# Kernel optimization log

Hardware: AMD Instinct MI355X
Metric: run time of the kernel (lower is better)

## Reference

```python
import jax, jax.numpy as jnp
import numpy as np

ALPHA = 0.2  # tf.nn.leaky_relu default

def leaky(x):
    return jnp.where(x >= 0, x, ALPHA * x)

def segment_softmax(score, seg, num_segments):
    m = jax.ops.segment_max(score, seg, num_segments=num_segments)
    e = jnp.exp(score - m[seg])
    denom = jax.ops.segment_sum(e, seg, num_segments=num_segments)
    return e / denom[seg]

def setup_inputs() -> dict:
    key = jax.random.key(0)
    ks = jax.random.split(key, 8)
    E, NE, NR, D, U = 500000, 100000, 1000, 128, 128
    return {
        "h_index": jax.random.randint(ks[0], (E,), 0, NE),
        "r_index": jax.random.randint(ks[1], (E,), 0, NR),
        "t_index": jax.random.randint(ks[2], (E,), 0, NE),
        "entity_embeddings": jax.random.normal(ks[3], (NE, D), jnp.float32),
        "relation_embeddings": jax.random.normal(ks[4], (NR, D), jnp.float32),
        "W": jax.random.normal(ks[5], (3 * D, U), jnp.float32) * 0.05,
        "a": jax.random.normal(ks[6], (U, 1), jnp.float32) * 0.1,
        "a_b": jnp.zeros((1,), jnp.float32),
        "bias": jnp.zeros((U,), jnp.float32),
    }

def reference(h_index, r_index, t_index, entity_embeddings, relation_embeddings, W, a, a_b, bias):
    num_entities = entity_embeddings.shape[0]
    h = entity_embeddings[h_index]          # [E, D]
    r = relation_embeddings[r_index]        # [E, D]
    t = entity_embeddings[t_index]          # [E, D]
    feats = jnp.concatenate([h, r, t], axis=-1) @ W  # [E, U]
    # att_kernel Dense(1, activation=leaky_relu), then wrapped again in att_activation
    score = leaky(leaky(feats @ a + a_b))[:, 0]      # [E]
    alpha = segment_softmax(score, h_index, num_entities)
    msg = feats * alpha[:, None]                     # gcn_mapper: edge features * weight
    reduced = jax.ops.segment_sum(msg, h_index, num_segments=num_entities)  # [NE, U]
    out = reduced + bias                             # identity_updater returns reduced_msg
    return jax.nn.relu(out)
```

## Files before the change

kernel.cpp:

```cpp
#include <hip/hip_runtime.h>
#include <hip/hip_bf16.h>

#define ALPHA2 0.04f

typedef __attribute__((ext_vector_type(8))) short short8;
typedef __attribute__((ext_vector_type(4))) float floatx4;
typedef __attribute__((ext_vector_type(8))) unsigned short ushort8;

__device__ __forceinline__ unsigned short f2bf(float f) {
    unsigned u = __float_as_uint(f);
    unsigned r = (u + 0x7fffu + ((u >> 16) & 1u)) >> 16;
    return (unsigned short)r;
}
__device__ __forceinline__ float bf2f(unsigned short h) {
    return __uint_as_float((unsigned)h << 16);
}

__global__ void k_prep(const float* __restrict__ W, unsigned short* __restrict__ Wt,
                       int* __restrict__ count, int* __restrict__ cursor, int NE) {
    int idx = blockIdx.x * blockDim.x + threadIdx.x;
    if (idx < 384 * 128) {
        int k = idx >> 7, n = idx & 127;
        Wt[n * 384 + k] = f2bf(W[idx]);
    }
    if (idx < NE) { count[idx] = 0; cursor[idx] = 0; }
}

#define LDA 136

__device__ __forceinline__ void gemm_phase(
        const unsigned short* Ash, const unsigned short* Wsh,
        int rowbase, int nrows, int wave, int lane,
        const float* __restrict__ avec,
        unsigned short* __restrict__ OutB, float* __restrict__ svec) {
    int m16 = lane & 15, quad = lane >> 4;
    int rs = wave * 32;

    floatx4 acc[2][8];
    #pragma unroll
    for (int i = 0; i < 2; ++i)
        #pragma unroll
        for (int j = 0; j < 8; ++j) acc[i][j] = (floatx4){0.f, 0.f, 0.f, 0.f};

    #pragma unroll
    for (int kc = 0; kc < 4; ++kc) {
        short8 af[2], bf[8];
        #pragma unroll
        for (int i = 0; i < 2; ++i)
            af[i] = *(const short8*)(Ash + (rs + i * 16 + m16) * LDA + kc * 32 + quad * 8);
        #pragma unroll
        for (int j = 0; j < 8; ++j)
            bf[j] = *(const short8*)(Wsh + (j * 16 + m16) * LDA + kc * 32 + quad * 8);
        #pragma unroll
        for (int i = 0; i < 2; ++i)
            #pragma unroll
            for (int j = 0; j < 8; ++j)
                acc[i][j] = __builtin_amdgcn_mfma_f32_16x16x32_bf16(af[i], bf[j], acc[i][j], 0, 0, 0);
    }

    float av[8];
    #pragma unroll
    for (int j = 0; j < 8; ++j) av[j] = avec[j * 16 + m16];
    #pragma unroll
    for (int i = 0; i < 2; ++i) {
        #pragma unroll
        for (int reg = 0; reg < 4; ++reg) {
            int row = rowbase + rs + i * 16 + quad * 4 + reg;
            bool ok = row < nrows;
            float part = 0.f;
            #pragma unroll
            for (int j = 0; j < 8; ++j) {
                float v = acc[i][j][reg];
                part = fmaf(v, av[j], part);
                if (ok) OutB[(size_t)row * 128 + j * 16 + m16] = f2bf(v);
            }
            #pragma unroll
            for (int off = 1; off < 16; off <<= 1) part += __shfl_xor(part, off);
            if (ok && m16 == 0) svec[row] = part;
        }
    }
}

template <bool TWO>
__global__ __launch_bounds__(256) void k_gemm(
        const float* __restrict__ In,
        const unsigned short* __restrict__ Wt,
        int woffA, unsigned short* __restrict__ OutA, float* __restrict__ svecA,
        int woffB, unsigned short* __restrict__ OutB, float* __restrict__ svecB,
        int nrows, const float* __restrict__ avec) {
    __shared__ unsigned short Ash[128 * LDA];
    __shared__ unsigned short Wsh[128 * LDA];
    int tid = threadIdx.x;
    int rowbase = blockIdx.x * 128;
    int wave = tid >> 6, lane = tid & 63;

    #pragma unroll
    for (int it = 0; it < 16; ++it) {
        int id = it * 256 + tid;
        int chunk = id & 31, row = id >> 5;
        int grow = rowbase + row;
        if (grow > nrows - 1) grow = nrows - 1;
        float4 v = *(const float4*)(In + (size_t)grow * 128 + chunk * 4);
        ushort4 u = make_ushort4(f2bf(v.x), f2bf(v.y), f2bf(v.z), f2bf(v.w));
        *(ushort4*)(Ash + row * LDA + chunk * 4) = u;
    }
    #pragma unroll
    for (int it = 0; it < 8; ++it) {
        int id = it * 256 + tid;
        int chunk = id & 15, n = id >> 4;
        uint4 v = *(const uint4*)(Wt + (size_t)n * 384 + woffA + chunk * 8);
        *(uint4*)(Wsh + n * LDA + chunk * 8) = v;
    }
    __syncthreads();
    gemm_phase(Ash, Wsh, rowbase, nrows, wave, lane, avec, OutA, svecA);

    if (TWO) {
        __syncthreads();
        #pragma unroll
        for (int it = 0; it < 8; ++it) {
            int id = it * 256 + tid;
            int chunk = id & 15, n = id >> 4;
            uint4 v = *(const uint4*)(Wt + (size_t)n * 384 + woffB + chunk * 8);
            *(uint4*)(Wsh + n * LDA + chunk * 8) = v;
        }
        __syncthreads();
        gemm_phase(Ash, Wsh, rowbase, nrows, wave, lane, avec, OutB, svecB);
    }
}

__global__ void k_count(const int* __restrict__ h, int* __restrict__ count, int E) {
    int e = blockIdx.x * blockDim.x + threadIdx.x;
    if (e < E) atomicAdd(count + h[e], 1);
}

__device__ __forceinline__ int block_incl_scan256(int s, int* sh, int t) {
    sh[t] = s; __syncthreads();
    #pragma unroll
    for (int off = 1; off < 256; off <<= 1) {
        int x = 0;
        if (t >= off) x = sh[t - off];
        __syncthreads();
        sh[t] += x;
        __syncthreads();
    }
    return sh[t];
}

__global__ __launch_bounds__(256) void k_scan_a(const int* __restrict__ count, int NE,
                                                int* __restrict__ bsum) {
    __shared__ int sh[256];
    int b = blockIdx.x, t = threadIdx.x;
    int base = b * 1024 + t * 4, s = 0;
    #pragma unroll
    for (int j = 0; j < 4; ++j) { int i = base + j; if (i < NE) s += count[i]; }
    sh[t] = s; __syncthreads();
    for (int off = 128; off > 0; off >>= 1) {
        if (t < off) sh[t] += sh[t + off];
        __syncthreads();
    }
    if (t == 0) bsum[b] = sh[0];
}

__global__ __launch_bounds__(256) void k_scan_b(int* __restrict__ bsum, int NB) {
    __shared__ int sh[256];
    int t = threadIdx.x;
    int v[4]; int s = 0;
    #pragma unroll
    for (int j = 0; j < 4; ++j) { int i = t * 4 + j; v[j] = (i < NB) ? bsum[i] : 0; s += v[j]; }
    int incl = block_incl_scan256(s, sh, t);
    int excl = incl - s;
    #pragma unroll
    for (int j = 0; j < 4; ++j) {
        int i = t * 4 + j;
        if (i < NB) { int tmp = v[j]; bsum[i] = excl; excl += tmp; }
    }
}

__global__ __launch_bounds__(256) void k_scan_c(const int* __restrict__ count, int NE,
                                                const int* __restrict__ bsum,
                                                int* __restrict__ rowstart, int E) {
    __shared__ int sh[256];
    int b = blockIdx.x, t = threadIdx.x;
    int base = b * 1024 + t * 4;
    int v[4]; int s = 0;
    #pragma unroll
    for (int j = 0; j < 4; ++j) { int i = base + j; v[j] = (i < NE) ? count[i] : 0; s += v[j]; }
    int incl = block_incl_scan256(s, sh, t);
    int excl = bsum[b] + incl - s;
    #pragma unroll
    for (int j = 0; j < 4; ++j) {
        int i = base + j;
        if (i < NE) { rowstart[i] = excl; excl += v[j]; }
    }
    if (b == 0 && t == 0) rowstart[NE] = E;
}

__global__ void k_score_scatter(const int* __restrict__ h, const int* __restrict__ r,
                                const int* __restrict__ t, const float* __restrict__ s1,
                                const float* __restrict__ s2, const float* __restrict__ s3,
                                const float* __restrict__ a_b,
                                const int* __restrict__ rowstart, int* __restrict__ cursor,
                                uint2* __restrict__ rt_s, int E) {
    int e = blockIdx.x * blockDim.x + threadIdx.x;
    if (e >= E) return;
    int hi = h[e], ri = r[e], ti = t[e];
    float x = s1[hi] + s2[ri] + s3[ti] + a_b[0];
    float sc = (x >= 0.f) ? x : ALPHA2 * x;
    float ev = __expf(sc);
    int pos = atomicAdd(cursor + hi, 1);
    rt_s[rowstart[hi] + pos] = make_uint2(((unsigned)ri << 17) | (unsigned)ti,
                                          __float_as_uint(ev));
}

__global__ __launch_bounds__(256) void k_aggregate(const int* __restrict__ rowstart,
                                                   const uint2* __restrict__ rt_s,
                                                   const unsigned short* __restrict__ Pb,
                                                   const unsigned short* __restrict__ Qb,
                                                   const unsigned short* __restrict__ Rb,
                                                   const float* __restrict__ bias,
                                                   float* __restrict__ out, int NE) {
    int gid = blockIdx.x * blockDim.x + threadIdx.x;
    int n = gid >> 4;
    int sl = gid & 15;
    if (n >= NE) return;
    int start = rowstart[n], end = rowstart[n + 1];
    int c0 = sl * 8;
    float acc[8] = {};
    float evsum = 0.f;
    int i = start;
    for (; i + 2 <= end; i += 2) {
        uint2 m0 = rt_s[i], m1 = rt_s[i + 1];
        float ev0 = __uint_as_float(m0.y), ev1 = __uint_as_float(m1.y);
        unsigned t0 = m0.x & 0x1FFFFu, r0 = m0.x >> 17;
        unsigned t1 = m1.x & 0x1FFFFu, r1 = m1.x >> 17;
        ushort8 q0 = *(const ushort8*)(Qb + (size_t)t0 * 128 + c0);
        ushort8 rr0 = *(const ushort8*)(Rb + (size_t)r0 * 128 + c0);
        ushort8 q1 = *(const ushort8*)(Qb + (size_t)t1 * 128 + c0);
        ushort8 rr1 = *(const ushort8*)(Rb + (size_t)r1 * 128 + c0);
        evsum += ev0 + ev1;
        #pragma unroll
        for (int j = 0; j < 8; ++j)
            acc[j] = fmaf(ev0, bf2f(q0[j]) + bf2f(rr0[j]), acc[j]);
        #pragma unroll
        for (int j = 0; j < 8; ++j)
            acc[j] = fmaf(ev1, bf2f(q1[j]) + bf2f(rr1[j]), acc[j]);
    }
    if (i < end) {
        uint2 m0 = rt_s[i];
        float ev0 = __uint_as_float(m0.y);
        unsigned t0 = m0.x & 0x1FFFFu, r0 = m0.x >> 17;
        ushort8 q0 = *(const ushort8*)(Qb + (size_t)t0 * 128 + c0);
        ushort8 rr0 = *(const ushort8*)(Rb + (size_t)r0 * 128 + c0);
        evsum += ev0;
        #pragma unroll
        for (int j = 0; j < 8; ++j)
            acc[j] = fmaf(ev0, bf2f(q0[j]) + bf2f(rr0[j]), acc[j]);
    }
    float4 b0 = *(const float4*)(bias + c0);
    float4 b1 = *(const float4*)(bias + c0 + 4);
    float bi[8] = {b0.x, b0.y, b0.z, b0.w, b1.x, b1.y, b1.z, b1.w};
    float o[8];
    if (end > start) {
        float inv = 1.f / evsum;
        ushort8 pb = *(const ushort8*)(Pb + (size_t)n * 128 + c0);
        #pragma unroll
        for (int j = 0; j < 8; ++j) o[j] = bf2f(pb[j]) + acc[j] * inv + bi[j];
    } else {
        #pragma unroll
        for (int j = 0; j < 8; ++j) o[j] = bi[j];
    }
    #pragma unroll
    for (int j = 0; j < 8; ++j) o[j] = fmaxf(o[j], 0.f);
    float* op = out + (size_t)n * 128 + c0;
    *(float4*)(op)     = make_float4(o[0], o[1], o[2], o[3]);
    *(float4*)(op + 4) = make_float4(o[4], o[5], o[6], o[7]);
}

static inline size_t align_up(size_t x, size_t a) { return (x + a - 1) / a * a; }

extern "C" void kernel_launch(void* const* d_in, const int* in_sizes, int n_in,
                              void* d_out, int out_size, void* d_ws, size_t ws_size,
                              hipStream_t stream) {
    const int* h_index = (const int*)d_in[0];
    const int* r_index = (const int*)d_in[1];
    const int* t_index = (const int*)d_in[2];
    const float* ent = (const float*)d_in[3];
    const float* rel = (const float*)d_in[4];
    const float* W = (const float*)d_in[5];
    const float* a = (const float*)d_in[6];
    const float* a_b = (const float*)d_in[7];
    const float* bias = (const float*)d_in[8];
    float* out = (float*)d_out;

    int E = in_sizes[0];
    int NE = in_sizes[3] / 128;
    int NR = in_sizes[4] / 128;

    char* p = (char*)d_ws;
    auto alloc = [&](size_t bytes) { char* q = p; p += align_up(bytes, 256); return (void*)q; };
    unsigned short* Pb = (unsigned short*)alloc((size_t)NE * 128 * 2);
    unsigned short* Qb = (unsigned short*)alloc((size_t)NE * 128 * 2);
    unsigned short* Rb = (unsigned short*)alloc((size_t)NR * 128 * 2);
    unsigned short* Wt = (unsigned short*)alloc((size_t)128 * 384 * 2);
    float* s1 = (float*)alloc((size_t)NE * 4);
    float* s3 = (float*)alloc((size_t)NE * 4);
    float* s2 = (float*)alloc((size_t)NR * 4);
    int* count = (int*)alloc((size_t)NE * 4);
    int* cursor = (int*)alloc((size_t)NE * 4);
    int* rowstart = (int*)alloc((size_t)(NE + 1) * 4);
    int NB = (NE + 1023) / 1024;
    int* bsum = (int*)alloc((size_t)NB * 4);
    uint2* rt_s = (uint2*)alloc((size_t)E * 8);
    (void)ws_size; (void)n_in; (void)out_size;

    int nprep = (NE > 384 * 128) ? NE : 384 * 128;
    k_prep<<<(nprep + 255) / 256, 256, 0, stream>>>(W, Wt, count, cursor, NE);
    k_count<<<(E + 255) / 256, 256, 0, stream>>>(h_index, count, E);
    k_gemm<true><<<(NE + 127) / 128, 256, 0, stream>>>(ent, Wt, 0, Pb, s1, 256, Qb, s3, NE, a);
    k_gemm<false><<<(NR + 127) / 128, 256, 0, stream>>>(rel, Wt, 128, Rb, s2, 0, nullptr, nullptr, NR, a);
    k_scan_a<<<NB, 256, 0, stream>>>(count, NE, bsum);
    k_scan_b<<<1, 256, 0, stream>>>(bsum, NB);
    k_scan_c<<<NB, 256, 0, stream>>>(count, NE, bsum, rowstart, E);
    k_score_scatter<<<(E + 255) / 256, 256, 0, stream>>>(h_index, r_index, t_index,
                                                         s1, s2, s3, a_b, rowstart,
                                                         cursor, rt_s, E);
    k_aggregate<<<(NE * 16 + 255) / 256, 256, 0, stream>>>(rowstart, rt_s, Pb, Qb, Rb,
                                                           bias, out, NE);
}
```

Before: 230.8 us.

## Stage GEMM output through LDS for coalesced stores; record per-edge rank in count pass

Measured after the change: 216.5 us. 1.07x faster.

```diff
diff --git a/kernel.cpp b/kernel.cpp
--- a/kernel.cpp
+++ b/kernel.cpp
@@ -17,20 +17,20 @@
 }
 
 __global__ void k_prep(const float* __restrict__ W, unsigned short* __restrict__ Wt,
-                       int* __restrict__ count, int* __restrict__ cursor, int NE) {
+                       int* __restrict__ count, int NE) {
     int idx = blockIdx.x * blockDim.x + threadIdx.x;
     if (idx < 384 * 128) {
         int k = idx >> 7, n = idx & 127;
         Wt[n * 384 + k] = f2bf(W[idx]);
     }
-    if (idx < NE) { count[idx] = 0; cursor[idx] = 0; }
+    if (idx < NE) count[idx] = 0;
 }
 
 #define LDA 136
 
 __device__ __forceinline__ void gemm_phase(
-        const unsigned short* Ash, const unsigned short* Wsh,
-        int rowbase, int nrows, int wave, int lane,
+        const unsigned short* Ash, unsigned short* Wsh,
+        int rowbase, int nrows, int wave, int lane, int tid,
         const float* __restrict__ avec,
         unsigned short* __restrict__ OutB, float* __restrict__ svec) {
     int m16 = lane & 15, quad = lane >> 4;
@@ -66,17 +66,34 @@
         #pragma unroll
         for (int reg = 0; reg < 4; ++reg) {
             int row = rowbase + rs + i * 16 + quad * 4 + reg;
-            bool ok = row < nrows;
             float part = 0.f;
             #pragma unroll
-            for (int j = 0; j < 8; ++j) {
-                float v = acc[i][j][reg];
-                part = fmaf(v, av[j], part);
-                if (ok) OutB[(size_t)row * 128 + j * 16 + m16] = f2bf(v);
-            }
+            for (int j = 0; j < 8; ++j) part = fmaf(acc[i][j][reg], av[j], part);
             #pragma unroll
             for (int off = 1; off < 16; off <<= 1) part += __shfl_xor(part, off);
-            if (ok && m16 == 0) svec[row] = part;
+            if (row < nrows && m16 == 0) svec[row] = part;
+        }
+    }
+
+    __syncthreads();
+    #pragma unroll
+    for (int i = 0; i < 2; ++i)
+        #pragma unroll
+        for (int reg = 0; reg < 4; ++reg) {
+            int lrow = rs + i * 16 + quad * 4 + reg;
+            #pragma unroll
+            for (int j = 0; j < 8; ++j)
+                Wsh[lrow * LDA + j * 16 + m16] = f2bf(acc[i][j][reg]);
+        }
+    __syncthreads();
+    #pragma unroll
+    for (int it = 0; it < 8; ++it) {
+        int id = it * 256 + tid;
+        int chunk = id & 15, row = id >> 4;
+        int grow = rowbase + row;
+        if (grow < nrows) {
+            ushort8 v = *(const ushort8*)(Wsh + row * LDA + chunk * 8);
+            *(ushort8*)(OutB + (size_t)grow * 128 + chunk * 8) = v;
         }
     }
 }
@@ -112,7 +129,7 @@
         *(uint4*)(Wsh + n * LDA + chunk * 8) = v;
     }
     __syncthreads();
-    gemm_phase(Ash, Wsh, rowbase, nrows, wave, lane, avec, OutA, svecA);
+    gemm_phase(Ash, Wsh, rowbase, nrows, wave, lane, tid, avec, OutA, svecA);
 
     if (TWO) {
         __syncthreads();
@@ -124,13 +141,14 @@
             *(uint4*)(Wsh + n * LDA + chunk * 8) = v;
         }
         __syncthreads();
-        gemm_phase(Ash, Wsh, rowbase, nrows, wave, lane, avec, OutB, svecB);
-    }
-}
-
-__global__ void k_count(const int* __restrict__ h, int* __restrict__ count, int E) {
+        gemm_phase(Ash, Wsh, rowbase, nrows, wave, lane, tid, avec, OutB, svecB);
+    }
+}
+
+__global__ void k_count(const int* __restrict__ h, int* __restrict__ count,
+                        int* __restrict__ rank, int E) {
     int e = blockIdx.x * blockDim.x + threadIdx.x;
-    if (e < E) atomicAdd(count + h[e], 1);
+    if (e < E) rank[e] = atomicAdd(count + h[e], 1);
 }
 
 __device__ __forceinline__ int block_incl_scan256(int s, int* sh, int t) {
@@ -199,7 +217,7 @@
                                 const int* __restrict__ t, const float* __restrict__ s1,
                                 const float* __restrict__ s2, const float* __restrict__ s3,
                                 const float* __restrict__ a_b,
-                                const int* __restrict__ rowstart, int* __restrict__ cursor,
+                                const int* __restrict__ rowstart, const int* __restrict__ rank,
                                 uint2* __restrict__ rt_s, int E) {
     int e = blockIdx.x * blockDim.x + threadIdx.x;
     if (e >= E) return;
@@ -207,9 +225,8 @@
     float x = s1[hi] + s2[ri] + s3[ti] + a_b[0];
     float sc = (x >= 0.f) ? x : ALPHA2 * x;
     float ev = __expf(sc);
-    int pos = atomicAdd(cursor + hi, 1);
-    rt_s[rowstart[hi] + pos] = make_uint2(((unsigned)ri << 17) | (unsigned)ti,
-                                          __float_as_uint(ev));
+    rt_s[rowstart[hi] + rank[e]] = make_uint2(((unsigned)ri << 17) | (unsigned)ti,
+                                              __float_as_uint(ev));
 }
 
 __global__ __launch_bounds__(256) void k_aggregate(const int* __restrict__ rowstart,
@@ -306,16 +323,16 @@
     float* s3 = (float*)alloc((size_t)NE * 4);
     float* s2 = (float*)alloc((size_t)NR * 4);
     int* count = (int*)alloc((size_t)NE * 4);
-    int* cursor = (int*)alloc((size_t)NE * 4);
     int* rowstart = (int*)alloc((size_t)(NE + 1) * 4);
+    int* rank = (int*)alloc((size_t)E * 4);
     int NB = (NE + 1023) / 1024;
     int* bsum = (int*)alloc((size_t)NB * 4);
     uint2* rt_s = (uint2*)alloc((size_t)E * 8);
     (void)ws_size; (void)n_in; (void)out_size;
 
     int nprep = (NE > 384 * 128) ? NE : 384 * 128;
-    k_prep<<<(nprep + 255) / 256, 256, 0, stream>>>(W, Wt, count, cursor, NE);
-    k_count<<<(E + 255) / 256, 256, 0, stream>>>(h_index, count, E);
+    k_prep<<<(nprep + 255) / 256, 256, 0, stream>>>(W, Wt, count, NE);
+    k_count<<<(E + 255) / 256, 256, 0, stream>>>(h_index, count, rank, E);
     k_gemm<true><<<(NE + 127) / 128, 256, 0, stream>>>(ent, Wt, 0, Pb, s1, 256, Qb, s3, NE, a);
     k_gemm<false><<<(NR + 127) / 128, 256, 0, stream>>>(rel, Wt, 128, Rb, s2, 0, nullptr, nullptr, NR, a);
     k_scan_a<<<NB, 256, 0, stream>>>(count, NE, bsum);
@@ -323,7 +340,7 @@
     k_scan_c<<<NB, 256, 0, stream>>>(count, NE, bsum, rowstart, E);
     k_score_scatter<<<(E + 255) / 256, 256, 0, stream>>>(h_index, r_index, t_index,
                                                          s1, s2, s3, a_b, rowstart,
-                                                         cursor, rt_s, E);
+                                                         rank, rt_s, E);
     k_aggregate<<<(NE * 16 + 255) / 256, 256, 0, stream>>>(rowstart, rt_s, Pb, Qb, Rb,
                                                            bias, out, NE);
 }
```
